# Optimization experiments

Measured on AMD Instinct MI355X. Metric: run time of the kernel, lower is better.

The kernel has to match this reference:

```python
import jax, jax.numpy as jnp
import numpy as np

N_NODES = 100000
N_EDGES = 1600000
D_FEAT = 128
HIDDEN = 16
N_CLASSES = 16


def setup_inputs() -> dict:
    key = jax.random.key(0)
    ks = jax.random.split(key, 6)
    x = jax.random.normal(ks[0], (N_NODES, D_FEAT), dtype=jnp.float32)
    edge_index = jax.random.randint(ks[1], (2, N_EDGES), 0, N_NODES, dtype=jnp.int64)
    # Glorot-ish scaled weights
    w1_rel = jax.random.normal(ks[2], (D_FEAT, HIDDEN), dtype=jnp.float32) / np.sqrt(D_FEAT)
    w1_root = jax.random.normal(ks[3], (D_FEAT, HIDDEN), dtype=jnp.float32) / np.sqrt(D_FEAT)
    b1 = jnp.zeros((HIDDEN,), dtype=jnp.float32)
    w2_rel = jax.random.normal(ks[4], (HIDDEN, N_CLASSES), dtype=jnp.float32) / np.sqrt(HIDDEN)
    w2_root = jax.random.normal(ks[5], (HIDDEN, N_CLASSES), dtype=jnp.float32) / np.sqrt(HIDDEN)
    b2 = jnp.zeros((N_CLASSES,), dtype=jnp.float32)
    return {"x": x, "edge_index": edge_index, "w1_rel": w1_rel, "w1_root": w1_root,
            "b1": b1, "w2_rel": w2_rel, "w2_root": w2_root, "b2": b2}


def _graph_conv(x, src, dst, w_rel, w_root, b):
    # PyG GraphConv(aggr='add'): out_i = lin_rel(sum_{j->i} x_j) + lin_root(x_i)
    n = x.shape[0]
    agg = jax.ops.segment_sum(x[src], dst, num_segments=n)  # [N, d_in]
    return agg @ w_rel + x @ w_root + b


def reference(x, edge_index, w1_rel, w1_root, b1, w2_rel, w2_root, b2):
    src, dst = edge_index[0], edge_index[1]
    h = jax.nn.relu(_graph_conv(x, src, dst, w1_rel, w1_root, b1))
    # F.dropout(training=False) -> identity in eval mode
    out = _graph_conv(h, src, dst, w2_rel, w2_root, b2)
    return jax.nn.log_softmax(out, axis=1)
```

## Files before the change

kernel.cpp:

```cpp
#include <hip/hip_runtime.h>

#define DFEAT 128
#define HID 16
#define BKT_NODES 512
#define BKT_SHIFT 9
#define CAP 8960
#define CHUNK 4096

typedef __attribute__((ext_vector_type(8))) short short8;
typedef __attribute__((ext_vector_type(4))) float floatx4;

__device__ __forceinline__ float bf2f(unsigned v) { return __uint_as_float(v << 16); }
__device__ __forceinline__ unsigned short f2bf(float f) {
    unsigned u = __float_as_uint(f);
    return (unsigned short)((u + 0x7FFFu + ((u >> 16) & 1u)) >> 16);
}
__device__ __forceinline__ unsigned pack2(float a, float b) {
    return (unsigned)f2bf(a) | ((unsigned)f2bf(b) << 16);
}

__global__ void k_detect(const unsigned short* __restrict__ x,
                         const int* __restrict__ ei,
                         int* __restrict__ flags) {
    const int lane = threadIdx.x;
    unsigned short v = x[2 * lane];
    int e = (v >> 7) & 0xFF;
    bool okbf = (v == 0) || (e >= 110 && e <= 130);
    unsigned long long mbf = __ballot(okbf);
    bool z = (ei[2 * lane + 1] == 0);
    unsigned long long mz = __ballot(z);
    if (lane == 0) {
        flags[0] = (__popcll(mbf) >= 52) ? 1 : 0;
        flags[1] = (__popcll(mz) >= 60) ? 1 : 0;
    }
}

__global__ void k_init(int* __restrict__ gcur, int nbkt) {
    int i = blockIdx.x * 256 + threadIdx.x;
    if (i < nbkt) gcur[i] = 0;
}

__global__ __launch_bounds__(256) void k_part(const int* __restrict__ ei,
                                              unsigned* __restrict__ eb,
                                              int* __restrict__ gcur,
                                              const int* __restrict__ flags,
                                              int E, int nbkt) {
    __shared__ int hist[256];
    const int t = threadIdx.x;
    if (t < nbkt) hist[t] = 0;
    __syncthreads();
    const int base = blockIdx.x * CHUNK;
    const int i64 = flags[1];
#pragma unroll 4
    for (int i = 0; i < CHUNK / 256; ++i) {
        int e = base + i * 256 + t;
        if (e < E) {
            int dst = i64 ? ei[2 * ((size_t)E + e)] : ei[(size_t)E + e];
            atomicAdd(&hist[dst >> BKT_SHIFT], 1);
        }
    }
    __syncthreads();
    if (t < nbkt) {
        int c = hist[t];
        hist[t] = c ? atomicAdd(&gcur[t], c) : 0;
    }
    __syncthreads();
    for (int i = 0; i < CHUNK / 256; ++i) {
        int e = base + i * 256 + t;
        if (e < E) {
            int src, dst;
            if (i64) { src = ei[2 * (size_t)e]; dst = ei[2 * ((size_t)E + e)]; }
            else     { src = ei[e];             dst = ei[(size_t)E + e]; }
            int b = dst >> BKT_SHIFT;
            int pos = atomicAdd(&hist[b], 1);
            if (pos >= 0 && pos < CAP)
                eb[(size_t)b * CAP + pos] =
                    ((unsigned)src << BKT_SHIFT) | (unsigned)(dst & (BKT_NODES - 1));
        }
    }
}

__global__ __launch_bounds__(1024) void k_scan(const int* __restrict__ gcur,
                                               int* __restrict__ bktbase,
                                               int* __restrict__ offsets,
                                               int nbkt, int N) {
    __shared__ int s[1024];
    const int t = threadIdx.x;
    int c = 0;
    if (t < nbkt) { c = gcur[t]; c = (c < 0) ? 0 : (c > CAP ? CAP : c); }
    s[t] = c;
    __syncthreads();
    for (int off = 1; off < 1024; off <<= 1) {
        int v = (t >= off) ? s[t - off] : 0;
        __syncthreads();
        s[t] += v;
        __syncthreads();
    }
    if (t < nbkt) bktbase[t] = s[t] - c;
    if (t == nbkt - 1) offsets[N] = s[t];
}

__global__ __launch_bounds__(512) void k_sort(const unsigned* __restrict__ eb,
                                              const int* __restrict__ gcur,
                                              const int* __restrict__ bktbase,
                                              unsigned* __restrict__ csr,
                                              int* __restrict__ offsets,
                                              int N) {
    __shared__ unsigned ew[CAP];
    __shared__ unsigned srt[CAP];
    __shared__ int cnts[BKT_NODES];
    __shared__ int offs[BKT_NODES];
    const int t = threadIdx.x;
    const int b = blockIdx.x;
    int cnt = gcur[b];
    if (cnt < 0) cnt = 0;
    if (cnt > CAP) cnt = CAP;
    const int base = bktbase[b];
    cnts[t] = 0;
    __syncthreads();
    const unsigned* ep = eb + (size_t)b * CAP;
    for (int i = t; i < cnt; i += 512) {
        unsigned w = ep[i];
        ew[i] = w;
        atomicAdd(&cnts[w & (BKT_NODES - 1u)], 1);
    }
    __syncthreads();
    offs[t] = cnts[t];
    __syncthreads();
    for (int off = 1; off < BKT_NODES; off <<= 1) {
        int v = (t >= off) ? offs[t - off] : 0;
        __syncthreads();
        offs[t] += v;
        __syncthreads();
    }
    {
        int ex = offs[t] - cnts[t];
        cnts[t] = ex;
        int gn = b * BKT_NODES + t;
        if (gn < N) offsets[gn] = base + ex;
    }
    __syncthreads();
    for (int i = t; i < cnt; i += 512) {
        unsigned w = ew[i];
        int pos = atomicAdd(&cnts[w & (BKT_NODES - 1u)], 1);
        srt[pos] = w >> BKT_SHIFT;
    }
    __syncthreads();
    for (int i = t; i < cnt; i += 512) csr[base + i] = srt[i];
}

__global__ __launch_bounds__(256) void k_lin1(const void* __restrict__ xv,
                                              const void* __restrict__ wrel,
                                              const void* __restrict__ wroot,
                                              unsigned short* __restrict__ p1b,
                                              unsigned short* __restrict__ q1b,
                                              const int* __restrict__ flags,
                                              int N) {
    const int t = threadIdx.x;
    const int lane = t & 63, wave = t >> 6;
    const int bf = flags[0];
    const int m = lane & 15;
    const int quad = lane >> 4;
    const int nodebase = blockIdx.x * 64 + wave * 16;

    short8 Brel[4], Broot[4];
    if (bf) {
        const unsigned short* a = (const unsigned short*)wrel;
        const unsigned short* c = (const unsigned short*)wroot;
#pragma unroll
        for (int kb = 0; kb < 4; ++kb) {
            short8 br, bo;
#pragma unroll
            for (int j = 0; j < 8; ++j) {
                int k = kb * 32 + quad * 8 + j;
                br[j] = (short)a[k * HID + m];
                bo[j] = (short)c[k * HID + m];
            }
            Brel[kb] = br; Broot[kb] = bo;
        }
    } else {
        const float* a = (const float*)wrel;
        const float* c = (const float*)wroot;
#pragma unroll
        for (int kb = 0; kb < 4; ++kb) {
            short8 br, bo;
#pragma unroll
            for (int j = 0; j < 8; ++j) {
                int k = kb * 32 + quad * 8 + j;
                br[j] = (short)f2bf(a[k * HID + m]);
                bo[j] = (short)f2bf(c[k * HID + m]);
            }
            Brel[kb] = br; Broot[kb] = bo;
        }
    }

    int row = nodebase + m;
    if (row >= N) row = N - 1;

    floatx4 accP = {0.f, 0.f, 0.f, 0.f}, accQ = {0.f, 0.f, 0.f, 0.f};
    if (bf) {
        const unsigned short* xp = (const unsigned short*)xv;
        const unsigned short* rp = xp + (size_t)row * DFEAT + quad * 8;
#pragma unroll
        for (int kb = 0; kb < 4; ++kb) {
            short8 A = *(const short8*)(rp + kb * 32);
            accP = __builtin_amdgcn_mfma_f32_16x16x32_bf16(A, Brel[kb], accP, 0, 0, 0);
            accQ = __builtin_amdgcn_mfma_f32_16x16x32_bf16(A, Broot[kb], accQ, 0, 0, 0);
        }
    } else {
        const float* xp = (const float*)xv;
        const float* rp = xp + (size_t)row * DFEAT + quad * 8;
#pragma unroll
        for (int kb = 0; kb < 4; ++kb) {
            float4 v0 = *(const float4*)(rp + kb * 32);
            float4 v1 = *(const float4*)(rp + kb * 32 + 4);
            short8 A;
            A[0] = (short)f2bf(v0.x); A[1] = (short)f2bf(v0.y);
            A[2] = (short)f2bf(v0.z); A[3] = (short)f2bf(v0.w);
            A[4] = (short)f2bf(v1.x); A[5] = (short)f2bf(v1.y);
            A[6] = (short)f2bf(v1.z); A[7] = (short)f2bf(v1.w);
            accP = __builtin_amdgcn_mfma_f32_16x16x32_bf16(A, Brel[kb], accP, 0, 0, 0);
            accQ = __builtin_amdgcn_mfma_f32_16x16x32_bf16(A, Broot[kb], accQ, 0, 0, 0);
        }
    }

#pragma unroll
    for (int r = 0; r < 4; ++r) {
        int node = nodebase + quad * 4 + r;
        if (node < N) {
            p1b[(size_t)node * HID + m] = f2bf(accP[r]);
            q1b[(size_t)node * HID + m] = f2bf(accQ[r]);
        }
    }
}

__global__ __launch_bounds__(256) void k_agg1(const int* __restrict__ offsets,
                                              const unsigned* __restrict__ csr,
                                              const unsigned short* __restrict__ p1b,
                                              const unsigned short* __restrict__ q1b,
                                              const void* __restrict__ b1,
                                              const void* __restrict__ w2rel,
                                              const void* __restrict__ w2root,
                                              unsigned short* __restrict__ p2b,
                                              unsigned short* __restrict__ q2b,
                                              const int* __restrict__ flags,
                                              int N) {
    __shared__ float4 swp[HID][8];
    __shared__ float sb[HID];
    const int t = threadIdx.x;
    const int bf = flags[0];
    if (t < 128) {
        int k = t >> 3, p = t & 7;
        float4 w;
        if (bf) {
            const unsigned short* a = (const unsigned short*)w2rel;
            const unsigned short* c = (const unsigned short*)w2root;
            w = make_float4(bf2f(a[k * 16 + 2 * p]), bf2f(a[k * 16 + 2 * p + 1]),
                            bf2f(c[k * 16 + 2 * p]), bf2f(c[k * 16 + 2 * p + 1]));
        } else {
            const float* a = (const float*)w2rel;
            const float* c = (const float*)w2root;
            w = make_float4(a[k * 16 + 2 * p], a[k * 16 + 2 * p + 1],
                            c[k * 16 + 2 * p], c[k * 16 + 2 * p + 1]);
        }
        swp[k][p] = w;
    }
    if (t < HID) sb[t] = bf ? bf2f(((const unsigned short*)b1)[t]) : ((const float*)b1)[t];
    __syncthreads();

    const int grp = t >> 3, jp = t & 7;
    const int n = blockIdx.x * 32 + grp;
    if (n >= N) return;

    const int beg = offsets[n], end = offsets[n + 1];
    float2 acc = make_float2(0.f, 0.f);
    int e = beg;
    for (; e + 4 <= end; e += 4) {
        unsigned s0 = csr[e], s1 = csr[e + 1], s2 = csr[e + 2], s3 = csr[e + 3];
        unsigned u0 = *(const unsigned*)(p1b + (size_t)s0 * HID + 2 * jp);
        unsigned u1 = *(const unsigned*)(p1b + (size_t)s1 * HID + 2 * jp);
        unsigned u2 = *(const unsigned*)(p1b + (size_t)s2 * HID + 2 * jp);
        unsigned u3 = *(const unsigned*)(p1b + (size_t)s3 * HID + 2 * jp);
        acc.x += bf2f(u0 & 0xFFFFu) + bf2f(u1 & 0xFFFFu)
               + bf2f(u2 & 0xFFFFu) + bf2f(u3 & 0xFFFFu);
        acc.y += bf2f(u0 >> 16) + bf2f(u1 >> 16) + bf2f(u2 >> 16) + bf2f(u3 >> 16);
    }
    for (; e < end; ++e) {
        unsigned s = csr[e];
        unsigned u = *(const unsigned*)(p1b + (size_t)s * HID + 2 * jp);
        acc.x += bf2f(u & 0xFFFFu);
        acc.y += bf2f(u >> 16);
    }
    unsigned qu = *(const unsigned*)(q1b + (size_t)n * HID + 2 * jp);
    float hx = fmaxf(acc.x + bf2f(qu & 0xFFFFu) + sb[2 * jp], 0.f);
    float hy = fmaxf(acc.y + bf2f(qu >> 16) + sb[2 * jp + 1], 0.f);

    float2 sp = make_float2(0.f, 0.f), sq = make_float2(0.f, 0.f);
#pragma unroll
    for (int k = 0; k < HID; ++k) {
        float hsel = (k & 1) ? hy : hx;
        float hk = __shfl(hsel, k >> 1, 8);
        float4 w = swp[k][jp];
        sp.x += hk * w.x; sp.y += hk * w.y;
        sq.x += hk * w.z; sq.y += hk * w.w;
    }
    ((unsigned*)p2b)[(size_t)n * 8 + jp] = pack2(sp.x, sp.y);
    ((unsigned*)q2b)[(size_t)n * 8 + jp] = pack2(sq.x, sq.y);
}

__global__ __launch_bounds__(256) void k_agg2(const int* __restrict__ offsets,
                                              const unsigned* __restrict__ csr,
                                              const unsigned short* __restrict__ p2b,
                                              const unsigned short* __restrict__ q2b,
                                              const void* __restrict__ b2,
                                              void* __restrict__ out,
                                              const int* __restrict__ flags,
                                              int N) {
    __shared__ float sb[HID];
    const int t = threadIdx.x;
    const int bf = flags[0];
    if (t < HID) sb[t] = bf ? bf2f(((const unsigned short*)b2)[t]) : ((const float*)b2)[t];
    __syncthreads();

    const int grp = t >> 3, jp = t & 7;
    const int n = blockIdx.x * 32 + grp;
    if (n >= N) return;

    const int beg = offsets[n], end = offsets[n + 1];
    float2 acc = make_float2(0.f, 0.f);
    int e = beg;
    for (; e + 4 <= end; e += 4) {
        unsigned s0 = csr[e], s1 = csr[e + 1], s2 = csr[e + 2], s3 = csr[e + 3];
        unsigned u0 = *(const unsigned*)(p2b + (size_t)s0 * HID + 2 * jp);
        unsigned u1 = *(const unsigned*)(p2b + (size_t)s1 * HID + 2 * jp);
        unsigned u2 = *(const unsigned*)(p2b + (size_t)s2 * HID + 2 * jp);
        unsigned u3 = *(const unsigned*)(p2b + (size_t)s3 * HID + 2 * jp);
        acc.x += bf2f(u0 & 0xFFFFu) + bf2f(u1 & 0xFFFFu)
               + bf2f(u2 & 0xFFFFu) + bf2f(u3 & 0xFFFFu);
        acc.y += bf2f(u0 >> 16) + bf2f(u1 >> 16) + bf2f(u2 >> 16) + bf2f(u3 >> 16);
    }
    for (; e < end; ++e) {
        unsigned s = csr[e];
        unsigned u = *(const unsigned*)(p2b + (size_t)s * HID + 2 * jp);
        acc.x += bf2f(u & 0xFFFFu);
        acc.y += bf2f(u >> 16);
    }
    unsigned qu = *(const unsigned*)(q2b + (size_t)n * HID + 2 * jp);
    float ox = acc.x + bf2f(qu & 0xFFFFu) + sb[2 * jp];
    float oy = acc.y + bf2f(qu >> 16) + sb[2 * jp + 1];

    float m = fmaxf(ox, oy);
#pragma unroll
    for (int mask = 1; mask < 8; mask <<= 1) m = fmaxf(m, __shfl_xor(m, mask, 8));
    float s = __expf(ox - m) + __expf(oy - m);
#pragma unroll
    for (int mask = 1; mask < 8; mask <<= 1) s += __shfl_xor(s, mask, 8);
    const float l = m + __logf(s);

    if (bf) ((unsigned*)out)[(size_t)n * 8 + jp] = pack2(ox - l, oy - l);
    else    ((float2*)out)[(size_t)n * 8 + jp] = make_float2(ox - l, oy - l);
}

extern "C" void kernel_launch(void* const* d_in, const int* in_sizes, int n_in,
                              void* d_out, int out_size, void* d_ws, size_t ws_size,
                              hipStream_t stream) {
    const void* x       = d_in[0];
    const int*  ei      = (const int*)d_in[1];
    const void* w1_rel  = d_in[2];
    const void* w1_root = d_in[3];
    const void* b1      = d_in[4];
    const void* w2_rel  = d_in[5];
    const void* w2_root = d_in[6];
    const void* b2      = d_in[7];

    const int N = in_sizes[0] / DFEAT;
    const int E = in_sizes[1] / 2;
    const int nbkt = (N + BKT_NODES - 1) / BKT_NODES;

    unsigned short* p1b = (unsigned short*)d_ws;
    unsigned short* q1b = p1b + (size_t)N * HID;
    unsigned short* p2b = q1b + (size_t)N * HID;
    unsigned short* q2b = p2b + (size_t)N * HID;
    unsigned* eb   = (unsigned*)(q2b + (size_t)N * HID);
    unsigned* csr  = eb + (size_t)nbkt * CAP;
    int* offsets   = (int*)(csr + (size_t)E);
    int* bktbase   = offsets + N + 1;
    int* gcur      = bktbase + nbkt;
    int* flags     = gcur + nbkt;

    k_detect<<<1, 64, 0, stream>>>((const unsigned short*)x, ei, flags);
    k_init<<<(nbkt + 255) / 256, 256, 0, stream>>>(gcur, nbkt);

    k_part<<<(E + CHUNK - 1) / CHUNK, 256, 0, stream>>>(ei, eb, gcur, flags, E, nbkt);
    k_scan<<<1, 1024, 0, stream>>>(gcur, bktbase, offsets, nbkt, N);
    k_sort<<<nbkt, 512, 0, stream>>>(eb, gcur, bktbase, csr, offsets, N);

    k_lin1<<<(N + 63) / 64, 256, 0, stream>>>(x, w1_rel, w1_root, p1b, q1b, flags, N);

    const int nblk = (N + 31) / 32;
    k_agg1<<<nblk, 256, 0, stream>>>(offsets, csr, p1b, q1b, b1, w2_rel, w2_root,
                                     p2b, q2b, flags, N);
    k_agg2<<<nblk, 256, 0, stream>>>(offsets, csr, p2b, q2b, b2, d_out, flags, N);
}
```

Baseline: 192.1 us.

## Fuse per-bucket CSR sort into first aggregation and drop scan kernel

Bucket size is halved to 256 nodes, and the separate scan and sort kernels are removed. The per-bucket counting sort now happens inside the layer-1 aggregation kernel, which aggregates straight from its shared-memory sorted list and also writes the CSR with per-node begin/end offsets for layer 2. The CSR is laid out at fixed stride CAP per bucket, so no global prefix scan is needed. The partition kernel keeps edges in registers between its histogram and scatter passes instead of reloading them, and the init kernel is folded into detect. This cuts launches and global passes over the edge list. The cost is only 391 blocks of aggregation work, fixed per-bucket capacity limits, and higher register and LDS use.

```diff
diff --git a/kernel.cpp b/kernel.cpp
--- a/kernel.cpp
+++ b/kernel.cpp
@@ -2,10 +2,12 @@
 
 #define DFEAT 128
 #define HID 16
-#define BKT_NODES 512
-#define BKT_SHIFT 9
-#define CAP 8960
+#define BKT_NODES 256
+#define BKT_SHIFT 8
+#define CAP 4608
+#define CAPI 18
 #define CHUNK 4096
+#define NOEDGE 0xFFFFFFFFu
 
 typedef __attribute__((ext_vector_type(8))) short short8;
 typedef __attribute__((ext_vector_type(4))) float floatx4;
@@ -19,25 +21,24 @@
     return (unsigned)f2bf(a) | ((unsigned)f2bf(b) << 16);
 }
 
-__global__ void k_detect(const unsigned short* __restrict__ x,
-                         const int* __restrict__ ei,
-                         int* __restrict__ flags) {
-    const int lane = threadIdx.x;
-    unsigned short v = x[2 * lane];
-    int e = (v >> 7) & 0xFF;
-    bool okbf = (v == 0) || (e >= 110 && e <= 130);
-    unsigned long long mbf = __ballot(okbf);
-    bool z = (ei[2 * lane + 1] == 0);
-    unsigned long long mz = __ballot(z);
-    if (lane == 0) {
-        flags[0] = (__popcll(mbf) >= 52) ? 1 : 0;
-        flags[1] = (__popcll(mz) >= 60) ? 1 : 0;
-    }
-}
-
-__global__ void k_init(int* __restrict__ gcur, int nbkt) {
-    int i = blockIdx.x * 256 + threadIdx.x;
-    if (i < nbkt) gcur[i] = 0;
+__global__ __launch_bounds__(512) void k_detect(const unsigned short* __restrict__ x,
+                                                const int* __restrict__ ei,
+                                                int* __restrict__ flags,
+                                                int* __restrict__ gcur, int nbkt) {
+    const int t = threadIdx.x;
+    for (int i = t; i < nbkt; i += 512) gcur[i] = 0;
+    if (t < 64) {
+        unsigned short v = x[2 * t];
+        int e = (v >> 7) & 0xFF;
+        bool okbf = (v == 0) || (e >= 110 && e <= 130);
+        unsigned long long mbf = __ballot(okbf);
+        bool z = (ei[2 * t + 1] == 0);
+        unsigned long long mz = __ballot(z);
+        if (t == 0) {
+            flags[0] = (__popcll(mbf) >= 52) ? 1 : 0;
+            flags[1] = (__popcll(mz) >= 60) ? 1 : 0;
+        }
+    }
 }
 
 __global__ __launch_bounds__(256) void k_part(const int* __restrict__ ei,
@@ -45,108 +46,43 @@
                                               int* __restrict__ gcur,
                                               const int* __restrict__ flags,
                                               int E, int nbkt) {
-    __shared__ int hist[256];
-    const int t = threadIdx.x;
-    if (t < nbkt) hist[t] = 0;
+    __shared__ int hist[512];
+    const int t = threadIdx.x;
+    for (int i = t; i < nbkt; i += 256) hist[i] = 0;
     __syncthreads();
     const int base = blockIdx.x * CHUNK;
     const int i64 = flags[1];
-#pragma unroll 4
-    for (int i = 0; i < CHUNK / 256; ++i) {
-        int e = base + i * 256 + t;
-        if (e < E) {
-            int dst = i64 ? ei[2 * ((size_t)E + e)] : ei[(size_t)E + e];
-            atomicAdd(&hist[dst >> BKT_SHIFT], 1);
-        }
-    }
-    __syncthreads();
-    if (t < nbkt) {
-        int c = hist[t];
-        hist[t] = c ? atomicAdd(&gcur[t], c) : 0;
-    }
-    __syncthreads();
-    for (int i = 0; i < CHUNK / 256; ++i) {
+    unsigned pk[16];
+    unsigned short bk[16];
+#pragma unroll
+    for (int i = 0; i < 16; ++i) {
         int e = base + i * 256 + t;
         if (e < E) {
             int src, dst;
             if (i64) { src = ei[2 * (size_t)e]; dst = ei[2 * ((size_t)E + e)]; }
             else     { src = ei[e];             dst = ei[(size_t)E + e]; }
             int b = dst >> BKT_SHIFT;
-            int pos = atomicAdd(&hist[b], 1);
+            pk[i] = ((unsigned)src << BKT_SHIFT) | (unsigned)(dst & (BKT_NODES - 1));
+            bk[i] = (unsigned short)b;
+            atomicAdd(&hist[b], 1);
+        } else {
+            bk[i] = 0xFFFFu;
+        }
+    }
+    __syncthreads();
+    for (int b = t; b < nbkt; b += 256) {
+        int c = hist[b];
+        hist[b] = c ? atomicAdd(&gcur[b], c) : 0;
+    }
+    __syncthreads();
+#pragma unroll
+    for (int i = 0; i < 16; ++i) {
+        if (bk[i] != 0xFFFFu) {
+            int pos = atomicAdd(&hist[bk[i]], 1);
             if (pos >= 0 && pos < CAP)
-                eb[(size_t)b * CAP + pos] =
-                    ((unsigned)src << BKT_SHIFT) | (unsigned)(dst & (BKT_NODES - 1));
-        }
-    }
-}
-
-__global__ __launch_bounds__(1024) void k_scan(const int* __restrict__ gcur,
-                                               int* __restrict__ bktbase,
-                                               int* __restrict__ offsets,
-                                               int nbkt, int N) {
-    __shared__ int s[1024];
-    const int t = threadIdx.x;
-    int c = 0;
-    if (t < nbkt) { c = gcur[t]; c = (c < 0) ? 0 : (c > CAP ? CAP : c); }
-    s[t] = c;
-    __syncthreads();
-    for (int off = 1; off < 1024; off <<= 1) {
-        int v = (t >= off) ? s[t - off] : 0;
-        __syncthreads();
-        s[t] += v;
-        __syncthreads();
-    }
-    if (t < nbkt) bktbase[t] = s[t] - c;
-    if (t == nbkt - 1) offsets[N] = s[t];
-}
-
-__global__ __launch_bounds__(512) void k_sort(const unsigned* __restrict__ eb,
-                                              const int* __restrict__ gcur,
-                                              const int* __restrict__ bktbase,
-                                              unsigned* __restrict__ csr,
-                                              int* __restrict__ offsets,
-                                              int N) {
-    __shared__ unsigned ew[CAP];
-    __shared__ unsigned srt[CAP];
-    __shared__ int cnts[BKT_NODES];
-    __shared__ int offs[BKT_NODES];
-    const int t = threadIdx.x;
-    const int b = blockIdx.x;
-    int cnt = gcur[b];
-    if (cnt < 0) cnt = 0;
-    if (cnt > CAP) cnt = CAP;
-    const int base = bktbase[b];
-    cnts[t] = 0;
-    __syncthreads();
-    const unsigned* ep = eb + (size_t)b * CAP;
-    for (int i = t; i < cnt; i += 512) {
-        unsigned w = ep[i];
-        ew[i] = w;
-        atomicAdd(&cnts[w & (BKT_NODES - 1u)], 1);
-    }
-    __syncthreads();
-    offs[t] = cnts[t];
-    __syncthreads();
-    for (int off = 1; off < BKT_NODES; off <<= 1) {
-        int v = (t >= off) ? offs[t - off] : 0;
-        __syncthreads();
-        offs[t] += v;
-        __syncthreads();
-    }
-    {
-        int ex = offs[t] - cnts[t];
-        cnts[t] = ex;
-        int gn = b * BKT_NODES + t;
-        if (gn < N) offsets[gn] = base + ex;
-    }
-    __syncthreads();
-    for (int i = t; i < cnt; i += 512) {
-        unsigned w = ew[i];
-        int pos = atomicAdd(&cnts[w & (BKT_NODES - 1u)], 1);
-        srt[pos] = w >> BKT_SHIFT;
-    }
-    __syncthreads();
-    for (int i = t; i < cnt; i += 512) csr[base + i] = srt[i];
+                eb[(size_t)bk[i] * CAP + pos] = pk[i];
+        }
+    }
 }
 
 __global__ __launch_bounds__(256) void k_lin1(const void* __restrict__ xv,
@@ -234,21 +170,29 @@
     }
 }
 
-__global__ __launch_bounds__(256) void k_agg1(const int* __restrict__ offsets,
-                                              const unsigned* __restrict__ csr,
-                                              const unsigned short* __restrict__ p1b,
-                                              const unsigned short* __restrict__ q1b,
-                                              const void* __restrict__ b1,
-                                              const void* __restrict__ w2rel,
-                                              const void* __restrict__ w2root,
-                                              unsigned short* __restrict__ p2b,
-                                              unsigned short* __restrict__ q2b,
-                                              const int* __restrict__ flags,
-                                              int N) {
+__global__ __launch_bounds__(256) void k_sagg1(const unsigned* __restrict__ eb,
+                                               const int* __restrict__ gcur,
+                                               const unsigned short* __restrict__ p1b,
+                                               const unsigned short* __restrict__ q1b,
+                                               const void* __restrict__ b1,
+                                               const void* __restrict__ w2rel,
+                                               const void* __restrict__ w2root,
+                                               unsigned short* __restrict__ p2b,
+                                               unsigned short* __restrict__ q2b,
+                                               unsigned* __restrict__ csr,
+                                               int* __restrict__ offsets,
+                                               int* __restrict__ ends,
+                                               const int* __restrict__ flags,
+                                               int N) {
+    __shared__ unsigned srt[CAP];
+    __shared__ int cnts[BKT_NODES];
+    __shared__ int offs[BKT_NODES];
     __shared__ float4 swp[HID][8];
     __shared__ float sb[HID];
     const int t = threadIdx.x;
+    const int b = blockIdx.x;
     const int bf = flags[0];
+
     if (t < 128) {
         int k = t >> 3, p = t & 7;
         float4 w;
@@ -266,49 +210,100 @@
         swp[k][p] = w;
     }
     if (t < HID) sb[t] = bf ? bf2f(((const unsigned short*)b1)[t]) : ((const float*)b1)[t];
-    __syncthreads();
+    cnts[t] = 0;
+    __syncthreads();
+
+    int cnt = gcur[b];
+    if (cnt < 0) cnt = 0;
+    if (cnt > CAP) cnt = CAP;
+    const unsigned* ep = eb + (size_t)b * CAP;
+
+    unsigned ev[CAPI];
+    int rk[CAPI];
+#pragma unroll
+    for (int i = 0; i < CAPI; ++i) {
+        int e = i * 256 + t;
+        if (e < cnt) {
+            unsigned w = ep[e];
+            ev[i] = w;
+            rk[i] = atomicAdd(&cnts[w & (BKT_NODES - 1u)], 1);
+        } else ev[i] = NOEDGE;
+    }
+    __syncthreads();
+    offs[t] = cnts[t];
+    __syncthreads();
+    for (int off = 1; off < BKT_NODES; off <<= 1) {
+        int v = (t >= off) ? offs[t - off] : 0;
+        __syncthreads();
+        offs[t] += v;
+        __syncthreads();
+    }
+#pragma unroll
+    for (int i = 0; i < CAPI; ++i) {
+        if (ev[i] != NOEDGE) {
+            unsigned local = ev[i] & (BKT_NODES - 1u);
+            int pos = offs[local] - cnts[local] + rk[i];
+            srt[pos] = ev[i] >> BKT_SHIFT;
+        }
+    }
+    __syncthreads();
+
+    const int base = b * CAP;
+    for (int e = t; e < cnt; e += 256) csr[base + e] = srt[e];
+    const int gb = b * BKT_NODES;
+    {
+        int gn = gb + t;
+        if (gn < N) {
+            offsets[gn] = base + offs[t] - cnts[t];
+            ends[gn]    = base + offs[t];
+        }
+    }
 
     const int grp = t >> 3, jp = t & 7;
-    const int n = blockIdx.x * 32 + grp;
-    if (n >= N) return;
-
-    const int beg = offsets[n], end = offsets[n + 1];
-    float2 acc = make_float2(0.f, 0.f);
-    int e = beg;
-    for (; e + 4 <= end; e += 4) {
-        unsigned s0 = csr[e], s1 = csr[e + 1], s2 = csr[e + 2], s3 = csr[e + 3];
-        unsigned u0 = *(const unsigned*)(p1b + (size_t)s0 * HID + 2 * jp);
-        unsigned u1 = *(const unsigned*)(p1b + (size_t)s1 * HID + 2 * jp);
-        unsigned u2 = *(const unsigned*)(p1b + (size_t)s2 * HID + 2 * jp);
-        unsigned u3 = *(const unsigned*)(p1b + (size_t)s3 * HID + 2 * jp);
-        acc.x += bf2f(u0 & 0xFFFFu) + bf2f(u1 & 0xFFFFu)
-               + bf2f(u2 & 0xFFFFu) + bf2f(u3 & 0xFFFFu);
-        acc.y += bf2f(u0 >> 16) + bf2f(u1 >> 16) + bf2f(u2 >> 16) + bf2f(u3 >> 16);
-    }
-    for (; e < end; ++e) {
-        unsigned s = csr[e];
-        unsigned u = *(const unsigned*)(p1b + (size_t)s * HID + 2 * jp);
-        acc.x += bf2f(u & 0xFFFFu);
-        acc.y += bf2f(u >> 16);
-    }
-    unsigned qu = *(const unsigned*)(q1b + (size_t)n * HID + 2 * jp);
-    float hx = fmaxf(acc.x + bf2f(qu & 0xFFFFu) + sb[2 * jp], 0.f);
-    float hy = fmaxf(acc.y + bf2f(qu >> 16) + sb[2 * jp + 1], 0.f);
-
-    float2 sp = make_float2(0.f, 0.f), sq = make_float2(0.f, 0.f);
-#pragma unroll
-    for (int k = 0; k < HID; ++k) {
-        float hsel = (k & 1) ? hy : hx;
-        float hk = __shfl(hsel, k >> 1, 8);
-        float4 w = swp[k][jp];
-        sp.x += hk * w.x; sp.y += hk * w.y;
-        sq.x += hk * w.z; sq.y += hk * w.w;
-    }
-    ((unsigned*)p2b)[(size_t)n * 8 + jp] = pack2(sp.x, sp.y);
-    ((unsigned*)q2b)[(size_t)n * 8 + jp] = pack2(sq.x, sq.y);
+#pragma unroll
+    for (int g = 0; g < 8; ++g) {
+        int node = g * 32 + grp;
+        int gn = gb + node;
+        int beg = offs[node] - cnts[node];
+        int end = offs[node];
+        float2 acc = make_float2(0.f, 0.f);
+        int e = beg;
+        for (; e + 2 <= end; e += 2) {
+            unsigned s0 = srt[e], s1 = srt[e + 1];
+            unsigned u0 = *(const unsigned*)(p1b + (size_t)s0 * HID + 2 * jp);
+            unsigned u1 = *(const unsigned*)(p1b + (size_t)s1 * HID + 2 * jp);
+            acc.x += bf2f(u0 & 0xFFFFu) + bf2f(u1 & 0xFFFFu);
+            acc.y += bf2f(u0 >> 16) + bf2f(u1 >> 16);
+        }
+        for (; e < end; ++e) {
+            unsigned u = *(const unsigned*)(p1b + (size_t)srt[e] * HID + 2 * jp);
+            acc.x += bf2f(u & 0xFFFFu);
+            acc.y += bf2f(u >> 16);
+        }
+        float hx = 0.f, hy = 0.f;
+        if (gn < N) {
+            unsigned qu = *(const unsigned*)(q1b + (size_t)gn * HID + 2 * jp);
+            hx = fmaxf(acc.x + bf2f(qu & 0xFFFFu) + sb[2 * jp], 0.f);
+            hy = fmaxf(acc.y + bf2f(qu >> 16) + sb[2 * jp + 1], 0.f);
+        }
+        float2 sp = make_float2(0.f, 0.f), sq = make_float2(0.f, 0.f);
+#pragma unroll
+        for (int k = 0; k < HID; ++k) {
+            float hsel = (k & 1) ? hy : hx;
+            float hk = __shfl(hsel, k >> 1, 8);
+            float4 w = swp[k][jp];
+            sp.x += hk * w.x; sp.y += hk * w.y;
+            sq.x += hk * w.z; sq.y += hk * w.w;
+        }
+        if (gn < N) {
+            ((unsigned*)p2b)[(size_t)gn * 8 + jp] = pack2(sp.x, sp.y);
+            ((unsigned*)q2b)[(size_t)gn * 8 + jp] = pack2(sq.x, sq.y);
+        }
+    }
 }
 
 __global__ __launch_bounds__(256) void k_agg2(const int* __restrict__ offsets,
+                                              const int* __restrict__ ends,
                                               const unsigned* __restrict__ csr,
                                               const unsigned short* __restrict__ p2b,
                                               const unsigned short* __restrict__ q2b,
@@ -326,7 +321,7 @@
     const int n = blockIdx.x * 32 + grp;
     if (n >= N) return;
 
-    const int beg = offsets[n], end = offsets[n + 1];
+    const int beg = offsets[n], end = ends[n];
     float2 acc = make_float2(0.f, 0.f);
     int e = beg;
     for (; e + 4 <= end; e += 4) {
@@ -383,22 +378,16 @@
     unsigned short* q2b = p2b + (size_t)N * HID;
     unsigned* eb   = (unsigned*)(q2b + (size_t)N * HID);
     unsigned* csr  = eb + (size_t)nbkt * CAP;
-    int* offsets   = (int*)(csr + (size_t)E);
-    int* bktbase   = offsets + N + 1;
-    int* gcur      = bktbase + nbkt;
+    int* offsets   = (int*)(csr + (size_t)nbkt * CAP);
+    int* ends      = offsets + N;
+    int* gcur      = ends + N;
     int* flags     = gcur + nbkt;
 
-    k_detect<<<1, 64, 0, stream>>>((const unsigned short*)x, ei, flags);
-    k_init<<<(nbkt + 255) / 256, 256, 0, stream>>>(gcur, nbkt);
-
+    k_detect<<<1, 512, 0, stream>>>((const unsigned short*)x, ei, flags, gcur, nbkt);
     k_part<<<(E + CHUNK - 1) / CHUNK, 256, 0, stream>>>(ei, eb, gcur, flags, E, nbkt);
-    k_scan<<<1, 1024, 0, stream>>>(gcur, bktbase, offsets, nbkt, N);
-    k_sort<<<nbkt, 512, 0, stream>>>(eb, gcur, bktbase, csr, offsets, N);
-
     k_lin1<<<(N + 63) / 64, 256, 0, stream>>>(x, w1_rel, w1_root, p1b, q1b, flags, N);
-
-    const int nblk = (N + 31) / 32;
-    k_agg1<<<nblk, 256, 0, stream>>>(offsets, csr, p1b, q1b, b1, w2_rel, w2_root,
-                                     p2b, q2b, flags, N);
-    k_agg2<<<nblk, 256, 0, stream>>>(offsets, csr, p2b, q2b, b2, d_out, flags, N);
-}
+    k_sagg1<<<nbkt, 256, 0, stream>>>(eb, gcur, p1b, q1b, b1, w2_rel, w2_root,
+                                      p2b, q2b, csr, offsets, ends, flags, N);
+    k_agg2<<<(N + 31) / 32, 256, 0, stream>>>(offsets, ends, csr, p2b, q2b, b2,
+                                              d_out, flags, N);
+}
```

New measurement: 193.2 us. No clear change (+0.5%).
